# Performance work log

Measured on AMD Instinct MI355X. Metric: run time of the kernel, lower is better.

Reference implementation:

```python
import jax, jax.numpy as jnp
import numpy as np

N_NODES = 100000
N_EDGES = 1600000
IN_CH = 128
OUT_CH = 64
HID = 2 * OUT_CH  # 128


def setup_inputs() -> dict:
    key = jax.random.key(0)
    ks = jax.random.split(key, 8)
    x = jax.random.normal(ks[0], (N_NODES, IN_CH), dtype=jnp.float32)
    edge_index = jax.random.randint(ks[1], (2, N_EDGES), 0, N_NODES, dtype=jnp.int64)

    def glorot(k, shape):
        return jax.random.normal(k, shape, dtype=jnp.float32) / jnp.sqrt(jnp.float32(shape[0]))

    W1 = glorot(ks[2], (IN_CH, HID))
    b1 = jax.random.normal(ks[3], (HID,), dtype=jnp.float32) * 0.01
    W_mu = glorot(ks[4], (HID, OUT_CH))
    b_mu = jax.random.normal(ks[5], (OUT_CH,), dtype=jnp.float32) * 0.01
    W_logstd = glorot(ks[6], (HID, OUT_CH))
    b_logstd = jax.random.normal(ks[7], (OUT_CH,), dtype=jnp.float32) * 0.01
    return {"x": x, "edge_index": edge_index, "W1": W1, "b1": b1,
            "W_mu": W_mu, "b_mu": b_mu, "W_logstd": W_logstd, "b_logstd": b_logstd}


def _gcn_norm(edge_index, n_nodes):
    # PyG GCNConv: add self-loops, symmetric normalization deg^{-1/2} A deg^{-1/2}
    loop = jnp.arange(n_nodes, dtype=edge_index.dtype)
    src = jnp.concatenate([edge_index[0], loop])  # [E+N]
    dst = jnp.concatenate([edge_index[1], loop])  # [E+N]
    deg = jax.ops.segment_sum(jnp.ones_like(dst, dtype=jnp.float32), dst,
                              num_segments=n_nodes)
    dinv = jnp.where(deg > 0, jax.lax.rsqrt(jnp.maximum(deg, 1.0)), 0.0)
    norm = dinv[src] * dinv[dst]  # [E+N]
    return src, dst, norm


def _gcn_conv(x, src, dst, norm, W, b, n_nodes):
    h = x @ W                                   # [N, out] linear first (small out dims)
    msg = h[src] * norm[:, None]                # [E+N, out] gather + scale
    out = jax.ops.segment_sum(msg, dst, num_segments=n_nodes)  # scatter-add
    return out + b


def reference(x, edge_index, W1, b1, W_mu, b_mu, W_logstd, b_logstd):
    n = x.shape[0]
    src, dst, norm = _gcn_norm(edge_index, n)  # same graph for all three layers
    h = jax.nn.relu(_gcn_conv(x, src, dst, norm, W1, b1, n))
    mu = _gcn_conv(h, src, dst, norm, W_mu, b_mu, n)
    logstd = _gcn_conv(h, src, dst, norm, W_logstd, b_logstd, n)
    return mu, logstd
```

## Files before the change

kernel.cpp:

```cpp
#include <hip/hip_runtime.h>
#include <stdint.h>

#define N_NODES 100000
#define N_EDGES 1600000
#define BSHIFT 9
#define NB 196
#define CAP_T 9216
#define CAPP 11264
#define SENT 0x80000000u

typedef __attribute__((ext_vector_type(8))) short short8;
typedef __attribute__((ext_vector_type(4))) float f32x4;
typedef __attribute__((ext_vector_type(2))) float f32x2;
typedef __attribute__((ext_vector_type(4))) unsigned u32x4;
typedef __attribute__((ext_vector_type(2))) unsigned u32x2;
typedef __attribute__((ext_vector_type(4))) int i32x4;

static __device__ __forceinline__ unsigned short f2bf(float f){
  unsigned u = __float_as_uint(f);
  u += 0x7fffu + ((u >> 16) & 1u);
  return (unsigned short)(u >> 16);
}
static __device__ __forceinline__ unsigned pack2bf(float a, float b){
  return (unsigned)f2bf(a) | ((unsigned)f2bf(b) << 16);
}
static __device__ __forceinline__ void upk8(u32x2 r, f32x2 w, f32x2* acc){
  #pragma unroll
  for (int b = 0; b < 2; ++b){
    unsigned u = r[b];
    f32x2 p0, p1;
    p0.x = (float)(int)(signed char)(u);
    p0.y = (float)(int)(signed char)(u >> 8);
    p1.x = (float)(int)(signed char)(u >> 16);
    p1.y = (float)(int)(signed char)(u >> 24);
    acc[2*b]     = __builtin_elementwise_fma(w, p0, acc[2*b]);
    acc[2*b + 1] = __builtin_elementwise_fma(w, p1, acc[2*b + 1]);
  }
}

__global__ __launch_bounds__(256)
void k_init(const float* __restrict__ W1, const float* __restrict__ Wmu,
            const float* __restrict__ Wls, short8* __restrict__ img,
            unsigned* __restrict__ gcur, float* __restrict__ dsc1,
            float* __restrict__ dsc2){
  int t = threadIdx.x;
  if (blockIdx.x == 16){
    if (t < NB) gcur[t] = t * CAP_T;
    if (t == 0){ dsc1[N_NODES] = 0.f; dsc2[N_NODES] = 0.f; }
    return;
  }
  int gid = blockIdx.x*256 + t;
  int k = gid >> 11, slot = gid & 2047;
  int lane = slot & 63, ks = (slot >> 6) & 3, tt = slot >> 8;
  int c = tt*16 + (lane & 15);
  int kb = ks*32 + (lane >> 4)*8;
  short8 v;
  #pragma unroll
  for (int j = 0; j < 8; ++j){
    float f;
    if (k == 0) f = W1[(kb + j)*128 + c];
    else        f = (c < 64) ? Wmu[(kb + j)*64 + c] : Wls[(kb + j)*64 + (c - 64)];
    v[j] = (short)f2bf(f);
  }
  img[gid] = v;
}

__global__ __launch_bounds__(256)
void k_binB(const int* __restrict__ ei, unsigned* __restrict__ gcur,
            unsigned* __restrict__ tmp){
  __shared__ unsigned cnt[NB];
  __shared__ unsigned gbase[NB];
  __shared__ unsigned loff[NB];
  __shared__ unsigned sc[256];
  __shared__ unsigned sen[2048];
  __shared__ unsigned spos[2048];
  int t = threadIdx.x;
  for (int j = t; j < NB; j += 256) cnt[j] = 0u;
  __syncthreads();
  unsigned bk[8], rk[8], en[8];
  int e0 = blockIdx.x*2048 + t*8;
  #pragma unroll
  for (int half = 0; half < 2; ++half){
    i32x4 sv, dv;
    bool any = (e0 + half*4) < N_EDGES;
    if (any){
      sv = *(const i32x4*)(ei + e0 + half*4);
      dv = *(const i32x4*)(ei + N_EDGES + e0 + half*4);
    }
    #pragma unroll
    for (int j = 0; j < 4; ++j){
      int q = half*4 + j;
      int e = e0 + q;
      bool ok = e < N_EDGES;
      unsigned d = ok ? (unsigned)dv[j] : 0u;
      unsigned s = ok ? (unsigned)sv[j] : 0u;
      ok = ok && d < N_NODES && s < N_NODES;
      bk[q] = ok ? (d >> BSHIFT) : 0xffffffffu;
      rk[q] = 0u; en[q] = 0u;
      if (ok){ rk[q] = atomicAdd(&cnt[bk[q]], 1u); en[q] = s | ((d & 511u) << 17); }
    }
  }
  __syncthreads();
  sc[t] = (t < NB) ? cnt[t] : 0u;
  __syncthreads();
  for (int off = 1; off < 256; off <<= 1){
    unsigned a = (t >= off) ? sc[t - off] : 0u;
    __syncthreads();
    sc[t] += a;
    __syncthreads();
  }
  if (t < NB){
    loff[t]  = sc[t] - cnt[t];
    gbase[t] = cnt[t] ? atomicAdd(&gcur[t], cnt[t]) : 0u;
  }
  __syncthreads();
  unsigned total = sc[NB - 1];
  #pragma unroll
  for (int j = 0; j < 8; ++j)
    if (bk[j] != 0xffffffffu){
      unsigned lp = loff[bk[j]] + rk[j];
      unsigned gp = gbase[bk[j]] + rk[j];
      sen[lp]  = en[j];
      spos[lp] = (gp < (bk[j] + 1u)*CAP_T) ? gp : 0xffffffffu;
    }
  __syncthreads();
  for (unsigned idx = t; idx < total; idx += 256){
    unsigned p = spos[idx];
    if (p != 0xffffffffu) tmp[p] = sen[idx];
  }
}

__global__ __launch_bounds__(256)
void k_binC(const unsigned* __restrict__ gcur, const unsigned* __restrict__ tmp,
            unsigned* __restrict__ csr, unsigned* __restrict__ begdeg,
            float* __restrict__ dinv){
  __shared__ unsigned cnt[512];
  __shared__ unsigned cur[512];
  __shared__ unsigned sc[512];
  int b = blockIdx.x, t = threadIdx.x;
  unsigned base_t = (unsigned)b * CAP_T;
  unsigned basep  = (unsigned)b * CAPP;
  unsigned sz = min(gcur[b] - base_t, (unsigned)CAP_T);
  cnt[t] = 0u; cnt[t + 256] = 0u;
  __syncthreads();
  for (unsigned idx = t; idx < sz; idx += 256)
    atomicAdd(&cnt[(tmp[base_t + idx] >> 17) & 511u], 1u);
  __syncthreads();
  unsigned c0 = cnt[t], c1 = cnt[t + 256];
  unsigned p0 = (c0 + 7u) & ~7u, p1 = (c1 + 7u) & ~7u;
  sc[t] = p0; sc[t + 256] = p1;
  __syncthreads();
  for (int off = 1; off < 512; off <<= 1){
    unsigned a0 = (t >= off)       ? sc[t - off]       : 0u;
    unsigned a1 = (t + 256 >= off) ? sc[t + 256 - off] : 0u;
    __syncthreads();
    sc[t] += a0; sc[t + 256] += a1;
    __syncthreads();
  }
  unsigned e0 = sc[t] - p0, e1 = sc[t + 256] - p1;
  cur[t] = e0; cur[t + 256] = e1;
  {
    int n0 = b*512 + t, n1 = n0 + 256;
    if (n0 < N_NODES){
      begdeg[n0] = (((basep + e0) >> 3) << 11) | min(c0, 2047u);
      dinv[n0] = rsqrtf((float)(c0 + 1u));
      for (unsigned k = c0; k < p0; ++k) csr[basep + e0 + k] = SENT;
    }
    if (n1 < N_NODES){
      begdeg[n1] = (((basep + e1) >> 3) << 11) | min(c1, 2047u);
      dinv[n1] = rsqrtf((float)(c1 + 1u));
      for (unsigned k = c1; k < p1; ++k) csr[basep + e1 + k] = SENT;
    }
  }
  __syncthreads();
  for (unsigned idx = t; idx < sz; idx += 256){
    unsigned en = tmp[base_t + idx];
    unsigned p = atomicAdd(&cur[(en >> 17) & 511u], 1u);
    if (p < (unsigned)CAPP) csr[basep + p] = en;
  }
}

__global__ __launch_bounds__(256)
void k_pack(const unsigned* __restrict__ csr, unsigned* __restrict__ csr2){
  unsigned e = blockIdx.x*256 + threadIdx.x;
  if (e >= (unsigned)NB*CAPP) return;
  unsigned en = csr[e];
  csr2[e] = (en & SENT) ? (unsigned)N_NODES : (en & 0x1FFFFu);
}

template<bool AF32>
__global__ __launch_bounds__(256)
void k_gemm(const void* __restrict__ A_, const short8* __restrict__ img,
            signed char* __restrict__ out8, float* __restrict__ dscale,
            const float* __restrict__ dinv, int M)
{
  __shared__ short8 wf[2048];
  int tid = threadIdx.x;
  #pragma unroll
  for (int s = 0; s < 8; ++s) wf[tid + 256*s] = img[tid + 256*s];
  __syncthreads();

  int wave = tid >> 6, lane = tid & 63;
  int rb = blockIdx.x*128 + wave*32;
  int r0 = rb + (lane & 15);
  int r1 = r0 + 16;
  int ra0 = min(r0, M-1), ra1 = min(r1, M-1);
  int koff = (lane >> 4)*8;

  short8 a0[4], a1[4];
  if (AF32){
    const float* A = (const float*)A_;
    #pragma unroll
    for (int ks = 0; ks < 4; ++ks){
      const float* p0 = A + (size_t)ra0*128 + ks*32 + koff;
      const float* p1 = A + (size_t)ra1*128 + ks*32 + koff;
      f32x4 xa = *(const f32x4*)p0, xb = *(const f32x4*)(p0 + 4);
      f32x4 ya = *(const f32x4*)p1, yb = *(const f32x4*)(p1 + 4);
      short8 t0, t1;
      #pragma unroll
      for (int j = 0; j < 4; ++j){
        t0[j] = (short)f2bf(xa[j]); t0[j+4] = (short)f2bf(xb[j]);
        t1[j] = (short)f2bf(ya[j]); t1[j+4] = (short)f2bf(yb[j]);
      }
      a0[ks] = t0; a1[ks] = t1;
    }
  } else {
    const unsigned short* A = (const unsigned short*)A_;
    #pragma unroll
    for (int ks = 0; ks < 4; ++ks){
      a0[ks] = *(const short8*)(A + (size_t)ra0*128 + ks*32 + koff);
      a1[ks] = *(const short8*)(A + (size_t)ra1*128 + ks*32 + koff);
    }
  }

  f32x4 acc[2][8];
  #pragma unroll
  for (int t = 0; t < 8; ++t){ acc[0][t] = (f32x4)0.f; acc[1][t] = (f32x4)0.f; }

  #pragma unroll
  for (int t = 0; t < 8; ++t){
    #pragma unroll
    for (int ks = 0; ks < 4; ++ks){
      short8 b = wf[(t*4 + ks)*64 + lane];
      acc[0][t] = __builtin_amdgcn_mfma_f32_16x16x32_bf16(a0[ks], b, acc[0][t], 0, 0, 0);
      acc[1][t] = __builtin_amdgcn_mfma_f32_16x16x32_bf16(a1[ks], b, acc[1][t], 0, 0, 0);
    }
  }

  #pragma unroll
  for (int sub = 0; sub < 2; ++sub){
    #pragma unroll
    for (int j = 0; j < 4; ++j){
      float m = 0.f;
      #pragma unroll
      for (int t = 0; t < 8; ++t) m = fmaxf(m, fabsf(acc[sub][t][j]));
      #pragma unroll
      for (int off = 1; off < 16; off <<= 1) m = fmaxf(m, __shfl_xor(m, off));
      int r = rb + sub*16 + (lane >> 4)*4 + j;
      if (r < M){
        float inv = 127.f / fmaxf(m, 1e-20f);
        #pragma unroll
        for (int t = 0; t < 8; ++t){
          int q = __float2int_rn(acc[sub][t][j] * inv);
          q = max(-127, min(127, q));
          out8[(size_t)r*128 + t*16 + (lane & 15)] = (signed char)q;
        }
        if ((lane & 15) == 0) dscale[r] = dinv[r] * m * (1.f/127.f);
      }
    }
  }
}

template<int MODE>
__global__ __launch_bounds__(256)
void k_agg(const signed char* __restrict__ hin, const unsigned* __restrict__ begdeg,
           const unsigned* __restrict__ csr2, const float* __restrict__ dinv,
           const float* __restrict__ dscale,
           const float* __restrict__ bias, const float* __restrict__ bias2,
           unsigned* __restrict__ out_bf, float* __restrict__ out_f)
{
  int i = blockIdx.x*4 + (threadIdx.x >> 6);
  int lane = threadIdx.x & 63;
  int slot = lane >> 4, c8 = lane & 15;
  float di = dinv[i];

  f32x2 acc2[4];
  #pragma unroll
  for (int j = 0; j < 4; ++j){ acc2[j].x = 0.f; acc2[j].y = 0.f; }
  {
    u32x2 sv = *(const u32x2*)(hin + (size_t)i*128 + c8*8);
    float ws = (slot == 0) ? di * dscale[i] : 0.f;
    f32x2 wsv; wsv.x = ws; wsv.y = ws;
    upk8(sv, wsv, acc2);
  }

  unsigned pk = begdeg[i];
  unsigned beg = (pk >> 11) << 3;
  int nit = ((int)(pk & 2047u) + 7) >> 3;

  const u32x2* ep = (const u32x2*)(csr2 + beg + 2*slot);
  u32x2 eA = ep[0];
  u32x2 eB = ep[4];
  float dsA0 = dscale[eA[0]], dsA1 = dscale[eA[1]];
  u32x2 rA0 = *(const u32x2*)(hin + (size_t)eA[0]*128 + c8*8);
  u32x2 rA1 = *(const u32x2*)(hin + (size_t)eA[1]*128 + c8*8);

  for (int it = 0; it < nit; ++it){
    u32x2 eC = ep[4*it + 8];
    float dsB0 = dscale[eB[0]], dsB1 = dscale[eB[1]];
    u32x2 rB0 = *(const u32x2*)(hin + (size_t)eB[0]*128 + c8*8);
    u32x2 rB1 = *(const u32x2*)(hin + (size_t)eB[1]*128 + c8*8);

    f32x2 w0; w0.x = di * dsA0; w0.y = w0.x;
    f32x2 w1; w1.x = di * dsA1; w1.y = w1.x;
    upk8(rA0, w0, acc2);
    upk8(rA1, w1, acc2);

    eA = eB; eB = eC; dsA0 = dsB0; dsA1 = dsB1; rA0 = rB0; rA1 = rB1;
  }

  #pragma unroll
  for (int j = 0; j < 4; ++j){
    acc2[j].x += __shfl_xor(acc2[j].x, 16);
    acc2[j].x += __shfl_xor(acc2[j].x, 32);
    acc2[j].y += __shfl_xor(acc2[j].y, 16);
    acc2[j].y += __shfl_xor(acc2[j].y, 32);
  }

  if (slot != 0) return;
  int c0 = c8*8;
  if (MODE == 0){
    u32x4 o;
    #pragma unroll
    for (int j = 0; j < 4; ++j){
      float lo = fmaxf(acc2[j].x + bias[c0 + 2*j],     0.f);
      float hi = fmaxf(acc2[j].y + bias[c0 + 2*j + 1], 0.f);
      o[j] = pack2bf(lo, hi);
    }
    *(u32x4*)(out_bf + (size_t)i*64 + c8*4) = o;
  } else {
    const float* bsrc = (c8 < 8) ? (bias + c0) : (bias2 + (c0 - 64));
    float* base = (c8 < 8) ? (out_f + (size_t)i*64 + c0)
                           : (out_f + (size_t)N_NODES*64 + (size_t)i*64 + (c0 - 64));
    f32x4 o0, o1;
    o0[0] = acc2[0].x + bsrc[0]; o0[1] = acc2[0].y + bsrc[1];
    o0[2] = acc2[1].x + bsrc[2]; o0[3] = acc2[1].y + bsrc[3];
    o1[0] = acc2[2].x + bsrc[4]; o1[1] = acc2[2].y + bsrc[5];
    o1[2] = acc2[3].x + bsrc[6]; o1[3] = acc2[3].y + bsrc[7];
    __builtin_nontemporal_store(o0, (f32x4*)base);
    __builtin_nontemporal_store(o1, (f32x4*)(base + 4));
  }
}


extern "C" void kernel_launch(void* const* d_in, const int* in_sizes, int n_in,
                              void* d_out, int out_size, void* d_ws, size_t ws_size,
                              hipStream_t stream)
{
  const float* x   = (const float*)d_in[0];
  const int*   ei  = (const int*)d_in[1];
  const float* W1  = (const float*)d_in[2];
  const float* b1  = (const float*)d_in[3];
  const float* Wmu = (const float*)d_in[4];
  const float* bmu = (const float*)d_in[5];
  const float* Wls = (const float*)d_in[6];
  const float* bls = (const float*)d_in[7];
  float* out = (float*)d_out;

  char* ws = (char*)d_ws;
  unsigned*    begdeg = (unsigned*)ws;  ws += 400128;
  float*       dinv   = (float*)ws;     ws += 400128;
  float*       dsc1   = (float*)ws;     ws += 400128;
  float*       dsc2   = (float*)ws;     ws += 400128;
  unsigned*    gcur   = (unsigned*)ws;  ws += 1024;
  short8*      imgW   = (short8*)ws;    ws += 65536;
  unsigned*    csr    = (unsigned*)ws;  ws += (size_t)NB*CAPP*4;
  unsigned*    csr2   = (unsigned*)ws;  ws += (size_t)NB*CAPP*4 + 512;
  char*        shared = ws;             ws += 12800256;
  if (ws_size < (size_t)(ws - (char*)d_ws)) return;
  unsigned*    tmp  = (unsigned*)shared;
  signed char* bufA = (signed char*)shared;
  unsigned* bufB = (unsigned*)d_out;

  k_init<<<17, 256, 0, stream>>>(W1, Wmu, Wls, imgW, gcur, dsc1, dsc2);
  k_binB<<<(N_EDGES + 2047)/2048, 256, 0, stream>>>(ei, gcur, tmp);
  k_binC<<<NB, 256, 0, stream>>>(gcur, tmp, csr, begdeg, dinv);
  k_pack<<<(NB*CAPP + 255)/256, 256, 0, stream>>>(csr, csr2);

  k_gemm<true ><<<(N_NODES + 127)/128, 256, 0, stream>>>(x, imgW, bufA, dsc1, dinv, N_NODES);
  k_agg<0><<<N_NODES/4, 256, 0, stream>>>(bufA, begdeg, csr2, dinv, dsc1, b1, nullptr,
                                          bufB, nullptr);
  k_gemm<false><<<(N_NODES + 127)/128, 256, 0, stream>>>((unsigned short*)bufB, imgW + 2048,
                                                         bufA, dsc2, dinv, N_NODES);
  k_agg<1><<<N_NODES/4, 256, 0, stream>>>(bufA, begdeg, csr2, dinv, dsc2, bmu, bls,
                                          nullptr, out);
}
```

Before: 197.4 us.

## Fuse first GEMM with edge binning, drop pack kernel, widen aggregation loads

Runs the first-layer GEMM and the edge-binning pass as one heterogeneous launch, with separate block ranges sharing a single shared-memory buffer, so the two independent stages overlap. The GEMM now writes raw row scales, and the later CSR build multiplies them by dinv in place. The CSR build also writes compact source indices directly, removing the separate pack kernel and one intermediate array, at the cost of separate workspace for tmp and bufA. The aggregation kernel now uses 8 edge slots with 16-byte row loads and one edge per slot per iteration instead of two 8-byte loads, trading memory-level parallelism per lane for fewer, wider loads.

After: 205.2 us. 3.9% more time.

```diff
diff --git a/kernel.cpp b/kernel.cpp
--- a/kernel.cpp
+++ b/kernel.cpp
@@ -8,6 +8,8 @@
 #define CAP_T 9216
 #define CAPP 11264
 #define SENT 0x80000000u
+#define NGB 782
+#define NBB 782
 
 typedef __attribute__((ext_vector_type(8))) short short8;
 typedef __attribute__((ext_vector_type(4))) float f32x4;
@@ -24,17 +26,17 @@
 static __device__ __forceinline__ unsigned pack2bf(float a, float b){
   return (unsigned)f2bf(a) | ((unsigned)f2bf(b) << 16);
 }
-static __device__ __forceinline__ void upk8(u32x2 r, f32x2 w, f32x2* acc){
-  #pragma unroll
-  for (int b = 0; b < 2; ++b){
-    unsigned u = r[b];
+static __device__ __forceinline__ void upk16(u32x4 r, f32x2 w, f32x2* acc){
+  #pragma unroll
+  for (int d = 0; d < 4; ++d){
+    unsigned u = r[d];
     f32x2 p0, p1;
     p0.x = (float)(int)(signed char)(u);
     p0.y = (float)(int)(signed char)(u >> 8);
     p1.x = (float)(int)(signed char)(u >> 16);
     p1.y = (float)(int)(signed char)(u >> 24);
-    acc[2*b]     = __builtin_elementwise_fma(w, p0, acc[2*b]);
-    acc[2*b + 1] = __builtin_elementwise_fma(w, p1, acc[2*b + 1]);
+    acc[2*d]     = __builtin_elementwise_fma(w, p0, acc[2*d]);
+    acc[2*d + 1] = __builtin_elementwise_fma(w, p1, acc[2*d + 1]);
   }
 }
 
@@ -42,10 +44,11 @@
 void k_init(const float* __restrict__ W1, const float* __restrict__ Wmu,
             const float* __restrict__ Wls, short8* __restrict__ img,
             unsigned* __restrict__ gcur, float* __restrict__ dsc1,
-            float* __restrict__ dsc2){
+            float* __restrict__ dsc2, unsigned* __restrict__ csr2){
   int t = threadIdx.x;
   if (blockIdx.x == 16){
     if (t < NB) gcur[t] = t * CAP_T;
+    if (t < 64) csr2[(size_t)NB*CAPP + t] = (unsigned)N_NODES;
     if (t == 0){ dsc1[N_NODES] = 0.f; dsc2[N_NODES] = 0.f; }
     return;
   }
@@ -65,143 +68,18 @@
   img[gid] = v;
 }
 
-__global__ __launch_bounds__(256)
-void k_binB(const int* __restrict__ ei, unsigned* __restrict__ gcur,
-            unsigned* __restrict__ tmp){
-  __shared__ unsigned cnt[NB];
-  __shared__ unsigned gbase[NB];
-  __shared__ unsigned loff[NB];
-  __shared__ unsigned sc[256];
-  __shared__ unsigned sen[2048];
-  __shared__ unsigned spos[2048];
-  int t = threadIdx.x;
-  for (int j = t; j < NB; j += 256) cnt[j] = 0u;
-  __syncthreads();
-  unsigned bk[8], rk[8], en[8];
-  int e0 = blockIdx.x*2048 + t*8;
-  #pragma unroll
-  for (int half = 0; half < 2; ++half){
-    i32x4 sv, dv;
-    bool any = (e0 + half*4) < N_EDGES;
-    if (any){
-      sv = *(const i32x4*)(ei + e0 + half*4);
-      dv = *(const i32x4*)(ei + N_EDGES + e0 + half*4);
-    }
-    #pragma unroll
-    for (int j = 0; j < 4; ++j){
-      int q = half*4 + j;
-      int e = e0 + q;
-      bool ok = e < N_EDGES;
-      unsigned d = ok ? (unsigned)dv[j] : 0u;
-      unsigned s = ok ? (unsigned)sv[j] : 0u;
-      ok = ok && d < N_NODES && s < N_NODES;
-      bk[q] = ok ? (d >> BSHIFT) : 0xffffffffu;
-      rk[q] = 0u; en[q] = 0u;
-      if (ok){ rk[q] = atomicAdd(&cnt[bk[q]], 1u); en[q] = s | ((d & 511u) << 17); }
-    }
-  }
-  __syncthreads();
-  sc[t] = (t < NB) ? cnt[t] : 0u;
-  __syncthreads();
-  for (int off = 1; off < 256; off <<= 1){
-    unsigned a = (t >= off) ? sc[t - off] : 0u;
-    __syncthreads();
-    sc[t] += a;
-    __syncthreads();
-  }
-  if (t < NB){
-    loff[t]  = sc[t] - cnt[t];
-    gbase[t] = cnt[t] ? atomicAdd(&gcur[t], cnt[t]) : 0u;
-  }
-  __syncthreads();
-  unsigned total = sc[NB - 1];
-  #pragma unroll
-  for (int j = 0; j < 8; ++j)
-    if (bk[j] != 0xffffffffu){
-      unsigned lp = loff[bk[j]] + rk[j];
-      unsigned gp = gbase[bk[j]] + rk[j];
-      sen[lp]  = en[j];
-      spos[lp] = (gp < (bk[j] + 1u)*CAP_T) ? gp : 0xffffffffu;
-    }
-  __syncthreads();
-  for (unsigned idx = t; idx < total; idx += 256){
-    unsigned p = spos[idx];
-    if (p != 0xffffffffu) tmp[p] = sen[idx];
-  }
-}
-
-__global__ __launch_bounds__(256)
-void k_binC(const unsigned* __restrict__ gcur, const unsigned* __restrict__ tmp,
-            unsigned* __restrict__ csr, unsigned* __restrict__ begdeg,
-            float* __restrict__ dinv){
-  __shared__ unsigned cnt[512];
-  __shared__ unsigned cur[512];
-  __shared__ unsigned sc[512];
-  int b = blockIdx.x, t = threadIdx.x;
-  unsigned base_t = (unsigned)b * CAP_T;
-  unsigned basep  = (unsigned)b * CAPP;
-  unsigned sz = min(gcur[b] - base_t, (unsigned)CAP_T);
-  cnt[t] = 0u; cnt[t + 256] = 0u;
-  __syncthreads();
-  for (unsigned idx = t; idx < sz; idx += 256)
-    atomicAdd(&cnt[(tmp[base_t + idx] >> 17) & 511u], 1u);
-  __syncthreads();
-  unsigned c0 = cnt[t], c1 = cnt[t + 256];
-  unsigned p0 = (c0 + 7u) & ~7u, p1 = (c1 + 7u) & ~7u;
-  sc[t] = p0; sc[t + 256] = p1;
-  __syncthreads();
-  for (int off = 1; off < 512; off <<= 1){
-    unsigned a0 = (t >= off)       ? sc[t - off]       : 0u;
-    unsigned a1 = (t + 256 >= off) ? sc[t + 256 - off] : 0u;
-    __syncthreads();
-    sc[t] += a0; sc[t + 256] += a1;
-    __syncthreads();
-  }
-  unsigned e0 = sc[t] - p0, e1 = sc[t + 256] - p1;
-  cur[t] = e0; cur[t + 256] = e1;
-  {
-    int n0 = b*512 + t, n1 = n0 + 256;
-    if (n0 < N_NODES){
-      begdeg[n0] = (((basep + e0) >> 3) << 11) | min(c0, 2047u);
-      dinv[n0] = rsqrtf((float)(c0 + 1u));
-      for (unsigned k = c0; k < p0; ++k) csr[basep + e0 + k] = SENT;
-    }
-    if (n1 < N_NODES){
-      begdeg[n1] = (((basep + e1) >> 3) << 11) | min(c1, 2047u);
-      dinv[n1] = rsqrtf((float)(c1 + 1u));
-      for (unsigned k = c1; k < p1; ++k) csr[basep + e1 + k] = SENT;
-    }
-  }
-  __syncthreads();
-  for (unsigned idx = t; idx < sz; idx += 256){
-    unsigned en = tmp[base_t + idx];
-    unsigned p = atomicAdd(&cur[(en >> 17) & 511u], 1u);
-    if (p < (unsigned)CAPP) csr[basep + p] = en;
-  }
-}
-
-__global__ __launch_bounds__(256)
-void k_pack(const unsigned* __restrict__ csr, unsigned* __restrict__ csr2){
-  unsigned e = blockIdx.x*256 + threadIdx.x;
-  if (e >= (unsigned)NB*CAPP) return;
-  unsigned en = csr[e];
-  csr2[e] = (en & SENT) ? (unsigned)N_NODES : (en & 0x1FFFFu);
-}
-
-template<bool AF32>
-__global__ __launch_bounds__(256)
-void k_gemm(const void* __restrict__ A_, const short8* __restrict__ img,
-            signed char* __restrict__ out8, float* __restrict__ dscale,
-            const float* __restrict__ dinv, int M)
-{
-  __shared__ short8 wf[2048];
-  int tid = threadIdx.x;
+template<bool AF32, bool MULDINV>
+static __device__ __forceinline__
+void gemm_body(const void* __restrict__ A_, const short8* __restrict__ img,
+               signed char* __restrict__ out8, float* __restrict__ scale,
+               const float* __restrict__ dinv, int M, short8* wf, int tid, int bid)
+{
   #pragma unroll
   for (int s = 0; s < 8; ++s) wf[tid + 256*s] = img[tid + 256*s];
   __syncthreads();
 
   int wave = tid >> 6, lane = tid & 63;
-  int rb = blockIdx.x*128 + wave*32;
+  int rb = bid*128 + wave*32;
   int r0 = rb + (lane & 15);
   int r1 = r0 + 16;
   int ra0 = min(r0, M-1), ra1 = min(r1, M-1);
@@ -265,9 +143,153 @@
           q = max(-127, min(127, q));
           out8[(size_t)r*128 + t*16 + (lane & 15)] = (signed char)q;
         }
-        if ((lane & 15) == 0) dscale[r] = dinv[r] * m * (1.f/127.f);
+        if ((lane & 15) == 0)
+          scale[r] = (MULDINV ? dinv[r] : 1.f) * m * (1.f/127.f);
       }
     }
+  }
+}
+
+static __device__ __forceinline__
+void binB_body(const int* __restrict__ ei, unsigned* __restrict__ gcur,
+               unsigned* __restrict__ tmp, char* smem, int t, int bb)
+{
+  unsigned* cnt   = (unsigned*)smem;
+  unsigned* gbase = (unsigned*)(smem + 784);
+  unsigned* loff  = (unsigned*)(smem + 1568);
+  unsigned* sc    = (unsigned*)(smem + 2368);
+  unsigned* sen   = (unsigned*)(smem + 3392);
+  unsigned* spos  = (unsigned*)(smem + 11584);
+
+  for (int j = t; j < NB; j += 256) cnt[j] = 0u;
+  __syncthreads();
+  unsigned bk[8], rk[8], en[8];
+  int e0 = bb*2048 + t*8;
+  #pragma unroll
+  for (int half = 0; half < 2; ++half){
+    i32x4 sv, dv;
+    bool any = (e0 + half*4) < N_EDGES;
+    if (any){
+      sv = *(const i32x4*)(ei + e0 + half*4);
+      dv = *(const i32x4*)(ei + N_EDGES + e0 + half*4);
+    }
+    #pragma unroll
+    for (int j = 0; j < 4; ++j){
+      int q = half*4 + j;
+      int e = e0 + q;
+      bool ok = e < N_EDGES;
+      unsigned d = ok ? (unsigned)dv[j] : 0u;
+      unsigned s = ok ? (unsigned)sv[j] : 0u;
+      ok = ok && d < N_NODES && s < N_NODES;
+      bk[q] = ok ? (d >> BSHIFT) : 0xffffffffu;
+      rk[q] = 0u; en[q] = 0u;
+      if (ok){ rk[q] = atomicAdd(&cnt[bk[q]], 1u); en[q] = s | ((d & 511u) << 17); }
+    }
+  }
+  __syncthreads();
+  sc[t] = (t < NB) ? cnt[t] : 0u;
+  __syncthreads();
+  for (int off = 1; off < 256; off <<= 1){
+    unsigned a = (t >= off) ? sc[t - off] : 0u;
+    __syncthreads();
+    sc[t] += a;
+    __syncthreads();
+  }
+  if (t < NB){
+    loff[t]  = sc[t] - cnt[t];
+    gbase[t] = cnt[t] ? atomicAdd(&gcur[t], cnt[t]) : 0u;
+  }
+  __syncthreads();
+  unsigned total = sc[NB - 1];
+  #pragma unroll
+  for (int j = 0; j < 8; ++j)
+    if (bk[j] != 0xffffffffu){
+      unsigned lp = loff[bk[j]] + rk[j];
+      unsigned gp = gbase[bk[j]] + rk[j];
+      sen[lp]  = en[j];
+      spos[lp] = (gp < (bk[j] + 1u)*CAP_T) ? gp : 0xffffffffu;
+    }
+  __syncthreads();
+  for (unsigned idx = t; idx < total; idx += 256){
+    unsigned p = spos[idx];
+    if (p != 0xffffffffu) tmp[p] = sen[idx];
+  }
+}
+
+__global__ __launch_bounds__(256)
+void k_gemm_bin(const float* __restrict__ x, const short8* __restrict__ img,
+                signed char* __restrict__ out8, float* __restrict__ rmax,
+                const int* __restrict__ ei, unsigned* __restrict__ gcur,
+                unsigned* __restrict__ tmp)
+{
+  __shared__ char smem[32768];
+  int t = threadIdx.x;
+  if (blockIdx.x < NGB)
+    gemm_body<true, false>(x, img, out8, rmax, nullptr, N_NODES, (short8*)smem, t, blockIdx.x);
+  else
+    binB_body(ei, gcur, tmp, smem, t, blockIdx.x - NGB);
+}
+
+__global__ __launch_bounds__(256)
+void k_gemm2(const unsigned short* __restrict__ A, const short8* __restrict__ img,
+             signed char* __restrict__ out8, float* __restrict__ dscale,
+             const float* __restrict__ dinv)
+{
+  __shared__ short8 wf[2048];
+  gemm_body<false, true>(A, img, out8, dscale, dinv, N_NODES, wf, threadIdx.x, blockIdx.x);
+}
+
+__global__ __launch_bounds__(256)
+void k_binC(const unsigned* __restrict__ gcur, const unsigned* __restrict__ tmp,
+            unsigned* __restrict__ csr2, unsigned* __restrict__ begdeg,
+            float* __restrict__ dinv, float* __restrict__ dsc1){
+  __shared__ unsigned cnt[512];
+  __shared__ unsigned cur[512];
+  __shared__ unsigned sc[512];
+  int b = blockIdx.x, t = threadIdx.x;
+  unsigned base_t = (unsigned)b * CAP_T;
+  unsigned basep  = (unsigned)b * CAPP;
+  unsigned sz = min(gcur[b] - base_t, (unsigned)CAP_T);
+  cnt[t] = 0u; cnt[t + 256] = 0u;
+  __syncthreads();
+  for (unsigned idx = t; idx < sz; idx += 256)
+    atomicAdd(&cnt[(tmp[base_t + idx] >> 17) & 511u], 1u);
+  __syncthreads();
+  unsigned c0 = cnt[t], c1 = cnt[t + 256];
+  unsigned p0 = (c0 + 7u) & ~7u, p1 = (c1 + 7u) & ~7u;
+  sc[t] = p0; sc[t + 256] = p1;
+  __syncthreads();
+  for (int off = 1; off < 512; off <<= 1){
+    unsigned a0 = (t >= off)       ? sc[t - off]       : 0u;
+    unsigned a1 = (t + 256 >= off) ? sc[t + 256 - off] : 0u;
+    __syncthreads();
+    sc[t] += a0; sc[t + 256] += a1;
+    __syncthreads();
+  }
+  unsigned e0 = sc[t] - p0, e1 = sc[t + 256] - p1;
+  cur[t] = e0; cur[t + 256] = e1;
+  {
+    int n0 = b*512 + t, n1 = n0 + 256;
+    if (n0 < N_NODES){
+      begdeg[n0] = (((basep + e0) >> 3) << 11) | min(c0, 2047u);
+      float dv = rsqrtf((float)(c0 + 1u));
+      dinv[n0] = dv;
+      dsc1[n0] *= dv;
+      for (unsigned k = c0; k < p0; ++k) csr2[basep + e0 + k] = (unsigned)N_NODES;
+    }
+    if (n1 < N_NODES){
+      begdeg[n1] = (((basep + e1) >> 3) << 11) | min(c1, 2047u);
+      float dv = rsqrtf((float)(c1 + 1u));
+      dinv[n1] = dv;
+      dsc1[n1] *= dv;
+      for (unsigned k = c1; k < p1; ++k) csr2[basep + e1 + k] = (unsigned)N_NODES;
+    }
+  }
+  __syncthreads();
+  for (unsigned idx = t; idx < sz; idx += 256){
+    unsigned en = tmp[base_t + idx];
+    unsigned p = atomicAdd(&cur[(en >> 17) & 511u], 1u);
+    if (p < (unsigned)CAPP) csr2[basep + p] = en & 0x1FFFFu;
   }
 }
 
@@ -281,74 +303,74 @@
 {
   int i = blockIdx.x*4 + (threadIdx.x >> 6);
   int lane = threadIdx.x & 63;
-  int slot = lane >> 4, c8 = lane & 15;
+  int slot = lane >> 3, c16 = lane & 7;
   float di = dinv[i];
 
-  f32x2 acc2[4];
-  #pragma unroll
-  for (int j = 0; j < 4; ++j){ acc2[j].x = 0.f; acc2[j].y = 0.f; }
+  f32x2 acc2[8];
+  #pragma unroll
+  for (int j = 0; j < 8; ++j){ acc2[j].x = 0.f; acc2[j].y = 0.f; }
   {
-    u32x2 sv = *(const u32x2*)(hin + (size_t)i*128 + c8*8);
+    u32x4 sv = *(const u32x4*)(hin + (size_t)i*128 + c16*16);
     float ws = (slot == 0) ? di * dscale[i] : 0.f;
-    f32x2 wsv; wsv.x = ws; wsv.y = ws;
-    upk8(sv, wsv, acc2);
+    f32x2 w; w.x = ws; w.y = ws;
+    upk16(sv, w, acc2);
   }
 
   unsigned pk = begdeg[i];
   unsigned beg = (pk >> 11) << 3;
   int nit = ((int)(pk & 2047u) + 7) >> 3;
 
-  const u32x2* ep = (const u32x2*)(csr2 + beg + 2*slot);
-  u32x2 eA = ep[0];
-  u32x2 eB = ep[4];
-  float dsA0 = dscale[eA[0]], dsA1 = dscale[eA[1]];
-  u32x2 rA0 = *(const u32x2*)(hin + (size_t)eA[0]*128 + c8*8);
-  u32x2 rA1 = *(const u32x2*)(hin + (size_t)eA[1]*128 + c8*8);
+  const unsigned* ep = csr2 + beg + slot;
+  unsigned sA = ep[0];
+  unsigned sB = ep[8];
+  float dsA = dscale[sA];
+  u32x4 rA = *(const u32x4*)(hin + (size_t)sA*128 + c16*16);
 
   for (int it = 0; it < nit; ++it){
-    u32x2 eC = ep[4*it + 8];
-    float dsB0 = dscale[eB[0]], dsB1 = dscale[eB[1]];
-    u32x2 rB0 = *(const u32x2*)(hin + (size_t)eB[0]*128 + c8*8);
-    u32x2 rB1 = *(const u32x2*)(hin + (size_t)eB[1]*128 + c8*8);
-
-    f32x2 w0; w0.x = di * dsA0; w0.y = w0.x;
-    f32x2 w1; w1.x = di * dsA1; w1.y = w1.x;
-    upk8(rA0, w0, acc2);
-    upk8(rA1, w1, acc2);
-
-    eA = eB; eB = eC; dsA0 = dsB0; dsA1 = dsB1; rA0 = rB0; rA1 = rB1;
-  }
-
-  #pragma unroll
-  for (int j = 0; j < 4; ++j){
+    unsigned sC = ep[8*it + 16];
+    float dsB = dscale[sB];
+    u32x4 rB = *(const u32x4*)(hin + (size_t)sB*128 + c16*16);
+    f32x2 w; w.x = di * dsA; w.y = w.x;
+    upk16(rA, w, acc2);
+    sA = sB; sB = sC; dsA = dsB; rA = rB;
+  }
+
+  #pragma unroll
+  for (int j = 0; j < 8; ++j){
+    acc2[j].x += __shfl_xor(acc2[j].x, 8);
+    acc2[j].y += __shfl_xor(acc2[j].y, 8);
     acc2[j].x += __shfl_xor(acc2[j].x, 16);
+    acc2[j].y += __shfl_xor(acc2[j].y, 16);
     acc2[j].x += __shfl_xor(acc2[j].x, 32);
-    acc2[j].y += __shfl_xor(acc2[j].y, 16);
     acc2[j].y += __shfl_xor(acc2[j].y, 32);
   }
 
   if (slot != 0) return;
-  int c0 = c8*8;
+  int c0 = c16*16;
   if (MODE == 0){
-    u32x4 o;
+    u32x4 o0, o1;
     #pragma unroll
     for (int j = 0; j < 4; ++j){
-      float lo = fmaxf(acc2[j].x + bias[c0 + 2*j],     0.f);
-      float hi = fmaxf(acc2[j].y + bias[c0 + 2*j + 1], 0.f);
-      o[j] = pack2bf(lo, hi);
-    }
-    *(u32x4*)(out_bf + (size_t)i*64 + c8*4) = o;
+      o0[j] = pack2bf(fmaxf(acc2[j].x   + bias[c0 + 2*j],     0.f),
+                      fmaxf(acc2[j].y   + bias[c0 + 2*j + 1], 0.f));
+      o1[j] = pack2bf(fmaxf(acc2[4+j].x + bias[c0 + 8 + 2*j],     0.f),
+                      fmaxf(acc2[4+j].y + bias[c0 + 8 + 2*j + 1], 0.f));
+    }
+    *(u32x4*)(out_bf + (size_t)i*64 + c16*8)     = o0;
+    *(u32x4*)(out_bf + (size_t)i*64 + c16*8 + 4) = o1;
   } else {
-    const float* bsrc = (c8 < 8) ? (bias + c0) : (bias2 + (c0 - 64));
-    float* base = (c8 < 8) ? (out_f + (size_t)i*64 + c0)
-                           : (out_f + (size_t)N_NODES*64 + (size_t)i*64 + (c0 - 64));
-    f32x4 o0, o1;
-    o0[0] = acc2[0].x + bsrc[0]; o0[1] = acc2[0].y + bsrc[1];
-    o0[2] = acc2[1].x + bsrc[2]; o0[3] = acc2[1].y + bsrc[3];
-    o1[0] = acc2[2].x + bsrc[4]; o1[1] = acc2[2].y + bsrc[5];
-    o1[2] = acc2[3].x + bsrc[6]; o1[3] = acc2[3].y + bsrc[7];
-    __builtin_nontemporal_store(o0, (f32x4*)base);
-    __builtin_nontemporal_store(o1, (f32x4*)(base + 4));
+    const float* bsrc = (c16 < 4) ? (bias + c0) : (bias2 + (c0 - 64));
+    float* base = (c16 < 4) ? (out_f + (size_t)i*64 + c0)
+                            : (out_f + (size_t)N_NODES*64 + (size_t)i*64 + (c0 - 64));
+    #pragma unroll
+    for (int g = 0; g < 4; ++g){
+      f32x4 o;
+      o[0] = acc2[2*g].x     + bsrc[4*g + 0];
+      o[1] = acc2[2*g].y     + bsrc[4*g + 1];
+      o[2] = acc2[2*g + 1].x + bsrc[4*g + 2];
+      o[3] = acc2[2*g + 1].y + bsrc[4*g + 3];
+      __builtin_nontemporal_store(o, (f32x4*)(base + 4*g));
+    }
   }
 }
 
@@ -374,24 +396,19 @@
   float*       dsc2   = (float*)ws;     ws += 400128;
   unsigned*    gcur   = (unsigned*)ws;  ws += 1024;
   short8*      imgW   = (short8*)ws;    ws += 65536;
-  unsigned*    csr    = (unsigned*)ws;  ws += (size_t)NB*CAPP*4;
-  unsigned*    csr2   = (unsigned*)ws;  ws += (size_t)NB*CAPP*4 + 512;
-  char*        shared = ws;             ws += 12800256;
+  unsigned*    csr2   = (unsigned*)ws;  ws += (size_t)NB*CAPP*4 + 256;
+  unsigned*    tmp    = (unsigned*)ws;  ws += (size_t)NB*CAP_T*4;
+  signed char* bufA   = (signed char*)ws; ws += 12800256;
   if (ws_size < (size_t)(ws - (char*)d_ws)) return;
-  unsigned*    tmp  = (unsigned*)shared;
-  signed char* bufA = (signed char*)shared;
   unsigned* bufB = (unsigned*)d_out;
 
-  k_init<<<17, 256, 0, stream>>>(W1, Wmu, Wls, imgW, gcur, dsc1, dsc2);
-  k_binB<<<(N_EDGES + 2047)/2048, 256, 0, stream>>>(ei, gcur, tmp);
-  k_binC<<<NB, 256, 0, stream>>>(gcur, tmp, csr, begdeg, dinv);
-  k_pack<<<(NB*CAPP + 255)/256, 256, 0, stream>>>(csr, csr2);
-
-  k_gemm<true ><<<(N_NODES + 127)/128, 256, 0, stream>>>(x, imgW, bufA, dsc1, dinv, N_NODES);
+  k_init<<<17, 256, 0, stream>>>(W1, Wmu, Wls, imgW, gcur, dsc1, dsc2, csr2);
+  k_gemm_bin<<<NGB + NBB, 256, 0, stream>>>(x, imgW, bufA, dsc1, ei, gcur, tmp);
+  k_binC<<<NB, 256, 0, stream>>>(gcur, tmp, csr2, begdeg, dinv, dsc1);
+
   k_agg<0><<<N_NODES/4, 256, 0, stream>>>(bufA, begdeg, csr2, dinv, dsc1, b1, nullptr,
                                           bufB, nullptr);
-  k_gemm<false><<<(N_NODES + 127)/128, 256, 0, stream>>>((unsigned short*)bufB, imgW + 2048,
-                                                         bufA, dsc2, dinv, N_NODES);
+  k_gemm2<<<NGB, 256, 0, stream>>>((unsigned short*)bufB, imgW + 2048, bufA, dsc2, dinv);
   k_agg<1><<<N_NODES/4, 256, 0, stream>>>(bufA, begdeg, csr2, dinv, dsc2, bmu, bls,
                                           nullptr, out);
 }
```
